# Performance work log

Hardware: AMD Instinct MI355X
Metric: run time of the kernel (lower is better)

Reference implementation:

```python
import jax, jax.numpy as jnp
import numpy as np

NUM_SEGMENTS = 4480  # BATCH_SIZE * MAX_ATOMS = 64 * 70
ATOM_DIM = 64
BOND_DIM = 16
N_EDGES = 65536


def setup_inputs() -> dict:
    key = jax.random.key(0)
    k1, k2, k3, k4 = jax.random.split(key, 4)
    atom_feat = jax.random.normal(k1, (NUM_SEGMENTS, ATOM_DIM), dtype=jnp.float32)
    bond_feat = jax.random.normal(k2, (N_EDGES, BOND_DIM), dtype=jnp.float32)
    pair_idx = jax.random.randint(k3, (N_EDGES, 2), 0, NUM_SEGMENTS, dtype=jnp.int64)
    # glorot-uniform style kernel, zero bias (as in add_weight initializers)
    limit = float(np.sqrt(6.0 / (BOND_DIM + ATOM_DIM ** 2)))
    kernel = jax.random.uniform(k4, (BOND_DIM, ATOM_DIM ** 2), dtype=jnp.float32,
                                minval=-limit, maxval=limit)
    bias = jnp.zeros((ATOM_DIM ** 2,), dtype=jnp.float32)
    return {"atom_feat": atom_feat, "bond_feat": bond_feat,
            "pair_idx": pair_idx, "kernel": kernel, "bias": bias}


def reference(atom_feat, bond_feat, pair_idx, kernel, bias):
    atom_dim = atom_feat.shape[-1]
    # dense projection of bond features -> per-edge transform matrices
    bond_transformed = bond_feat @ kernel + bias               # [E, D*D]
    bond_transformed = bond_transformed.reshape(-1, atom_dim, atom_dim)  # [E, D, D]
    # gather neighbor (source) atom features per edge
    neighbor_feat = jnp.take(atom_feat, pair_idx[:, 1].astype(jnp.int32), axis=0)  # [E, D]
    # per-edge matrix-vector product
    messages = jnp.einsum('eij,ej->ei', bond_transformed, neighbor_feat)  # [E, D]
    # scatter-add into destination atoms
    return jax.ops.segment_sum(messages, pair_idx[:, 0].astype(jnp.int32),
                               num_segments=NUM_SEGMENTS)  # [NUM_SEGMENTS, D]
```

## Files before the change

kernel.cpp:

```cpp
#include <hip/hip_runtime.h>
#include <hip/hip_bf16.h>

#define NSEG   4480
#define ADIM   64
#define BDIM   16
#define NEDGE  65536
#define UPITCH 1088
#define LPITCH 68
#define CAP    64

__device__ __forceinline__ float bf2f(unsigned int bits_hi16) {
    union { unsigned int i; float f; } c; c.i = bits_hi16; return c.f;
}
__device__ __forceinline__ unsigned short f2bf(float f) {
    union { float f; unsigned int i; } c; c.f = f;
    unsigned int x = c.i;
    x += 0x7fffu + ((x >> 16) & 1u);
    return (unsigned short)(x >> 16);
}

__global__ __launch_bounds__(256) void proj_kernel(
    const float* __restrict__ atom,
    const float* __restrict__ kern,
    const float* __restrict__ bias,
    unsigned short* __restrict__ U,
    float* __restrict__ out,
    int*   __restrict__ cnt)
{
    __shared__ float As[64 * LPITCH];
    __shared__ float Bs[64 * LPITCH];

    const int t      = threadIdx.x;
    const int bx     = blockIdx.x;
    const int by     = blockIdx.y;
    const int a_base = bx * 64;
    const int c_base = by * 64;

    if (by == 0) {
        int gid = bx * 256 + t;
        ((float4*)out)[gid] = make_float4(0.f, 0.f, 0.f, 0.f);
    } else if (by == 1) {
        int gid = bx * 256 + t;
        if (gid < NSEG / 4) ((int4*)cnt)[gid] = make_int4(0, 0, 0, 0);
    }

#pragma unroll
    for (int k = 0; k < 4; ++k) {
        int id  = t + k * 256;
        int row = id >> 4;
        int j0  = (id & 15) * 4;
        float4 v = *(const float4*)(atom + (size_t)(a_base + row) * ADIM + j0);
        As[(j0 + 0) * LPITCH + row] = v.x;
        As[(j0 + 1) * LPITCH + row] = v.y;
        As[(j0 + 2) * LPITCH + row] = v.z;
        As[(j0 + 3) * LPITCH + row] = v.w;
    }
#pragma unroll
    for (int k = 0; k < 4; ++k) {
        int id   = t + k * 256;
        int crow = id >> 4;
        int j0   = (id & 15) * 4;
        int c    = c_base + crow;
        const float* bsrc = (c < 1024)
            ? (kern + (size_t)(c & 15) * 4096 + (size_t)(c >> 4) * 64)
            : (bias + (size_t)(c - 1024) * 64);
        float4 v = *(const float4*)(bsrc + j0);
        Bs[(j0 + 0) * LPITCH + crow] = v.x;
        Bs[(j0 + 1) * LPITCH + crow] = v.y;
        Bs[(j0 + 2) * LPITCH + crow] = v.z;
        Bs[(j0 + 3) * LPITCH + crow] = v.w;
    }
    __syncthreads();

    const int tx = t & 15;
    const int ty = t >> 4;
    const int a0 = ty * 4;
    const int c0 = tx * 4;

    float acc[4][4] = {};
#pragma unroll 8
    for (int j = 0; j < 64; ++j) {
        float4 av = *(const float4*)(As + j * LPITCH + a0);
        float4 bv = *(const float4*)(Bs + j * LPITCH + c0);
        acc[0][0] = fmaf(av.x, bv.x, acc[0][0]);
        acc[0][1] = fmaf(av.x, bv.y, acc[0][1]);
        acc[0][2] = fmaf(av.x, bv.z, acc[0][2]);
        acc[0][3] = fmaf(av.x, bv.w, acc[0][3]);
        acc[1][0] = fmaf(av.y, bv.x, acc[1][0]);
        acc[1][1] = fmaf(av.y, bv.y, acc[1][1]);
        acc[1][2] = fmaf(av.y, bv.z, acc[1][2]);
        acc[1][3] = fmaf(av.y, bv.w, acc[1][3]);
        acc[2][0] = fmaf(av.z, bv.x, acc[2][0]);
        acc[2][1] = fmaf(av.z, bv.y, acc[2][1]);
        acc[2][2] = fmaf(av.z, bv.z, acc[2][2]);
        acc[2][3] = fmaf(av.z, bv.w, acc[2][3]);
        acc[3][0] = fmaf(av.w, bv.x, acc[3][0]);
        acc[3][1] = fmaf(av.w, bv.y, acc[3][1]);
        acc[3][2] = fmaf(av.w, bv.z, acc[3][2]);
        acc[3][3] = fmaf(av.w, bv.w, acc[3][3]);
    }

#pragma unroll
    for (int r = 0; r < 4; ++r) {
        ushort4 o;
        o.x = f2bf(acc[r][0]);
        o.y = f2bf(acc[r][1]);
        o.z = f2bf(acc[r][2]);
        o.w = f2bf(acc[r][3]);
        *(ushort4*)(U + (size_t)(a_base + a0 + r) * UPITCH + c_base + c0) = o;
    }
}

__global__ __launch_bounds__(256) void scatter_kernel(
    const int* __restrict__ pair, int* __restrict__ cnt, int* __restrict__ slot)
{
    int e   = blockIdx.x * 256 + threadIdx.x;
    int src = pair[(size_t)e * 2 + 1];
    int pos = atomicAdd(&cnt[src], 1);
    if (pos < CAP) slot[src * CAP + pos] = e;
}

__global__ __launch_bounds__(256) void edge_kernel(
    const float*          __restrict__ bond,
    const int*            __restrict__ pair,
    const unsigned short* __restrict__ U,
    const int*            __restrict__ cnt,
    const int*            __restrict__ slot,
    float*                __restrict__ out)
{
    const int t    = threadIdx.x;
    const int lane = t & 63;
    const int w    = t >> 6;
    const int s    = blockIdx.x;

    int n = cnt[s];
    if (n > CAP) n = CAP;
    if (w * 4 >= n) return;

    const unsigned short* urow = U + (size_t)s * UPITCH;
    const uint4* up = (const uint4*)(urow + lane * 16);
    uint4 u0 = up[0];
    uint4 u1 = up[1];
    unsigned int uw[8] = { u0.x, u0.y, u0.z, u0.w, u1.x, u1.y, u1.z, u1.w };
    float ub = bf2f(((unsigned int)urow[1024 + lane]) << 16);

    for (int k0 = w * 4; k0 < n; k0 += 16) {
        int e[4];
#pragma unroll
        for (int j = 0; j < 4; ++j) {
            int kk = k0 + j;
            if (kk > n - 1) kk = n - 1;
            int ee = slot[s * CAP + kk];
            e[j] = __builtin_amdgcn_readfirstlane(ee);
        }

        int   dst[4];
        float bb[4][16];
#pragma unroll
        for (int j = 0; j < 4; ++j) {
            dst[j] = pair[(size_t)e[j] * 2 + 0];
            const float4* bp = (const float4*)(bond + (size_t)e[j] * BDIM);
            float4 b0 = bp[0], b1 = bp[1], b2 = bp[2], b3 = bp[3];
            bb[j][0]  = b0.x; bb[j][1]  = b0.y; bb[j][2]  = b0.z; bb[j][3]  = b0.w;
            bb[j][4]  = b1.x; bb[j][5]  = b1.y; bb[j][6]  = b1.z; bb[j][7]  = b1.w;
            bb[j][8]  = b2.x; bb[j][9]  = b2.y; bb[j][10] = b2.z; bb[j][11] = b2.w;
            bb[j][12] = b3.x; bb[j][13] = b3.y; bb[j][14] = b3.z; bb[j][15] = b3.w;
        }

        float m[4];
#pragma unroll
        for (int j = 0; j < 4; ++j) {
            float mm = ub;
#pragma unroll
            for (int q = 0; q < 8; ++q) {
                float lo = bf2f(uw[q] << 16);
                float hi = bf2f(uw[q] & 0xffff0000u);
                mm = fmaf(lo, bb[j][2 * q],     mm);
                mm = fmaf(hi, bb[j][2 * q + 1], mm);
            }
            m[j] = mm;
        }

#pragma unroll
        for (int j = 0; j < 4; ++j) {
            if (k0 + j < n)
                atomicAdd(out + (size_t)dst[j] * ADIM + lane, m[j]);
        }
    }
}

extern "C" void kernel_launch(void* const* d_in, const int* in_sizes, int n_in,
                              void* d_out, int out_size, void* d_ws, size_t ws_size,
                              hipStream_t stream) {
    const float* atom = (const float*)d_in[0];
    const float* bond = (const float*)d_in[1];
    const int*   pair = (const int*)  d_in[2];
    const float* kern = (const float*)d_in[3];
    const float* bias = (const float*)d_in[4];

    float* out = (float*)d_out;

    char* ws = (char*)d_ws;
    unsigned short* U = (unsigned short*)ws;
    int* cnt  = (int*)(ws + (size_t)NSEG * UPITCH * 2);
    int* slot = cnt + NSEG;

    dim3 g1(NSEG / 64, UPITCH / 64);
    proj_kernel<<<g1, 256, 0, stream>>>(atom, kern, bias, U, out, cnt);

    scatter_kernel<<<NEDGE / 256, 256, 0, stream>>>(pair, cnt, slot);

    edge_kernel<<<NSEG, 256, 0, stream>>>(bond, pair, U, cnt, slot, out);
}
```

Baseline: 101.5 us.

## Replace float atomics with per-edge message buffer and destination-sorted gather reduction

Instead of atomically adding each edge message into the output, messages are written to a per-edge buffer. A second bucketing by destination lets a new reduce kernel sum each atom's messages without atomics and write the output directly, so the output zeroing is dropped. This removes float atomic contention but adds an extra kernel launch, a 16 MB message buffer round trip through memory, and a second atomic bucketing pass.

```diff
diff --git a/kernel.cpp b/kernel.cpp
--- a/kernel.cpp
+++ b/kernel.cpp
@@ -24,8 +24,7 @@
     const float* __restrict__ kern,
     const float* __restrict__ bias,
     unsigned short* __restrict__ U,
-    float* __restrict__ out,
-    int*   __restrict__ cnt)
+    int*   __restrict__ cnt2)
 {
     __shared__ float As[64 * LPITCH];
     __shared__ float Bs[64 * LPITCH];
@@ -36,12 +35,9 @@
     const int a_base = bx * 64;
     const int c_base = by * 64;
 
-    if (by == 0) {
+    if (by == 1) {
         int gid = bx * 256 + t;
-        ((float4*)out)[gid] = make_float4(0.f, 0.f, 0.f, 0.f);
-    } else if (by == 1) {
-        int gid = bx * 256 + t;
-        if (gid < NSEG / 4) ((int4*)cnt)[gid] = make_int4(0, 0, 0, 0);
+        if (gid < (2 * NSEG) / 4) ((int4*)cnt2)[gid] = make_int4(0, 0, 0, 0);
     }
 
 #pragma unroll
@@ -111,29 +107,33 @@
     }
 }
 
-__global__ __launch_bounds__(256) void scatter_kernel(
-    const int* __restrict__ pair, int* __restrict__ cnt, int* __restrict__ slot)
-{
-    int e   = blockIdx.x * 256 + threadIdx.x;
-    int src = pair[(size_t)e * 2 + 1];
-    int pos = atomicAdd(&cnt[src], 1);
-    if (pos < CAP) slot[src * CAP + pos] = e;
-}
-
-__global__ __launch_bounds__(256) void edge_kernel(
+__global__ __launch_bounds__(256) void scatter2_kernel(
+    const int* __restrict__ pair,
+    int* __restrict__ cnt_src, int* __restrict__ cnt_dst,
+    int* __restrict__ slot_src, int* __restrict__ slot_dst)
+{
+    int e = blockIdx.x * 256 + threadIdx.x;
+    int2 p = ((const int2*)pair)[e];
+    int ps = atomicAdd(&cnt_src[p.y], 1);
+    if (ps < CAP) slot_src[p.y * CAP + ps] = e;
+    int pd = atomicAdd(&cnt_dst[p.x], 1);
+    if (pd < CAP) slot_dst[p.x * CAP + pd] = e;
+}
+
+__global__ __launch_bounds__(256) void msg_kernel(
     const float*          __restrict__ bond,
     const int*            __restrict__ pair,
     const unsigned short* __restrict__ U,
-    const int*            __restrict__ cnt,
-    const int*            __restrict__ slot,
-    float*                __restrict__ out)
+    const int*            __restrict__ cnt_src,
+    const int*            __restrict__ slot_src,
+    float*                __restrict__ msg)
 {
     const int t    = threadIdx.x;
     const int lane = t & 63;
     const int w    = t >> 6;
     const int s    = blockIdx.x;
 
-    int n = cnt[s];
+    int n = cnt_src[s];
     if (n > CAP) n = CAP;
     if (w * 4 >= n) return;
 
@@ -150,15 +150,13 @@
         for (int j = 0; j < 4; ++j) {
             int kk = k0 + j;
             if (kk > n - 1) kk = n - 1;
-            int ee = slot[s * CAP + kk];
+            int ee = slot_src[s * CAP + kk];
             e[j] = __builtin_amdgcn_readfirstlane(ee);
         }
 
-        int   dst[4];
         float bb[4][16];
 #pragma unroll
         for (int j = 0; j < 4; ++j) {
-            dst[j] = pair[(size_t)e[j] * 2 + 0];
             const float4* bp = (const float4*)(bond + (size_t)e[j] * BDIM);
             float4 b0 = bp[0], b1 = bp[1], b2 = bp[2], b3 = bp[3];
             bb[j][0]  = b0.x; bb[j][1]  = b0.y; bb[j][2]  = b0.z; bb[j][3]  = b0.w;
@@ -167,7 +165,6 @@
             bb[j][12] = b3.x; bb[j][13] = b3.y; bb[j][14] = b3.z; bb[j][15] = b3.w;
         }
 
-        float m[4];
 #pragma unroll
         for (int j = 0; j < 4; ++j) {
             float mm = ub;
@@ -178,15 +175,45 @@
                 mm = fmaf(lo, bb[j][2 * q],     mm);
                 mm = fmaf(hi, bb[j][2 * q + 1], mm);
             }
-            m[j] = mm;
-        }
-
-#pragma unroll
-        for (int j = 0; j < 4; ++j) {
             if (k0 + j < n)
-                atomicAdd(out + (size_t)dst[j] * ADIM + lane, m[j]);
-        }
-    }
+                msg[(size_t)e[j] * ADIM + lane] = mm;
+        }
+    }
+}
+
+__global__ __launch_bounds__(256) void reduce_kernel(
+    const float* __restrict__ msg,
+    const int*   __restrict__ cnt_dst,
+    const int*   __restrict__ slot_dst,
+    float*       __restrict__ out)
+{
+    const int t    = threadIdx.x;
+    const int lane = t & 63;
+    const int d    = blockIdx.x * 4 + (t >> 6);
+
+    int n = cnt_dst[d];
+    if (n > CAP) n = CAP;
+
+    float acc = 0.f;
+    for (int k0 = 0; k0 < n; k0 += 4) {
+        int e[4];
+#pragma unroll
+        for (int j = 0; j < 4; ++j) {
+            int kk = k0 + j;
+            if (kk > n - 1) kk = n - 1;
+            int ee = slot_dst[d * CAP + kk];
+            e[j] = __builtin_amdgcn_readfirstlane(ee);
+        }
+        float v[4];
+#pragma unroll
+        for (int j = 0; j < 4; ++j)
+            v[j] = msg[(size_t)e[j] * ADIM + lane];
+#pragma unroll
+        for (int j = 0; j < 4; ++j)
+            if (k0 + j < n) acc += v[j];
+    }
+
+    out[(size_t)d * ADIM + lane] = acc;
 }
 
 extern "C" void kernel_launch(void* const* d_in, const int* in_sizes, int n_in,
@@ -202,13 +229,20 @@
 
     char* ws = (char*)d_ws;
     unsigned short* U = (unsigned short*)ws;
-    int* cnt  = (int*)(ws + (size_t)NSEG * UPITCH * 2);
-    int* slot = cnt + NSEG;
+    int* cnt2     = (int*)(ws + (size_t)NSEG * UPITCH * 2);
+    int* cnt_src  = cnt2;
+    int* cnt_dst  = cnt2 + NSEG;
+    int* slot_src = cnt2 + 2 * NSEG;
+    int* slot_dst = slot_src + NSEG * CAP;
+    float* msg    = (float*)(slot_dst + NSEG * CAP);
 
     dim3 g1(NSEG / 64, UPITCH / 64);
-    proj_kernel<<<g1, 256, 0, stream>>>(atom, kern, bias, U, out, cnt);
-
-    scatter_kernel<<<NEDGE / 256, 256, 0, stream>>>(pair, cnt, slot);
-
-    edge_kernel<<<NSEG, 256, 0, stream>>>(bond, pair, U, cnt, slot, out);
-}
+    proj_kernel<<<g1, 256, 0, stream>>>(atom, kern, bias, U, cnt2);
+
+    scatter2_kernel<<<NEDGE / 256, 256, 0, stream>>>(pair, cnt_src, cnt_dst,
+                                                     slot_src, slot_dst);
+
+    msg_kernel<<<NSEG, 256, 0, stream>>>(bond, pair, U, cnt_src, slot_src, msg);
+
+    reduce_kernel<<<NSEG / 4, 256, 0, stream>>>(msg, cnt_dst, slot_dst, out);
+}
```

Result: slower. 107.7 us (+6.1%).
